# Kernel optimization log

Hardware: AMD Instinct MI355X
Metric: run time of the kernel (lower is better)

Reference implementation:

```python
import jax, jax.numpy as jnp
import numpy as np

N_NODES = 50000
N_EDGES = 800000
IN_CH = 16
OUT_CH = 16


def setup_inputs() -> dict:
    key = jax.random.key(0)
    ks = jax.random.split(key, 12)
    s = lambda d: 1.0 / np.sqrt(d)
    return {
        "x": jax.random.normal(ks[0], (N_NODES, IN_CH), jnp.float32),
        "edge_index": jax.random.randint(ks[1], (2, N_EDGES), 0, N_NODES, jnp.int64),
        "edge_attr": jax.random.uniform(ks[2], (N_EDGES, 8), jnp.float32),
        "W1": jax.random.normal(ks[3], (8, 100), jnp.float32) * s(8),
        "b1": jnp.zeros((100,), jnp.float32),
        "W2": jax.random.normal(ks[4], (100, 100), jnp.float32) * s(100),
        "b2": jnp.zeros((100,), jnp.float32),
        "W3": jax.random.normal(ks[5], (100, 100), jnp.float32) * s(100),
        "b3": jnp.zeros((100,), jnp.float32),
        "W4": jax.random.normal(ks[6], (100, IN_CH * OUT_CH), jnp.float32) * s(100),
        "b4": jnp.zeros((IN_CH * OUT_CH,), jnp.float32),
        "root": jax.random.normal(ks[7], (IN_CH, OUT_CH), jnp.float32) * s(IN_CH),
        "bias": jnp.zeros((OUT_CH,), jnp.float32),
    }


def reference(x, edge_index, edge_attr, W1, b1, W2, b2, W3, b3, W4, b4, root, bias):
    src, dst = edge_index[0], edge_index[1]
    # edge MLP -> per-edge weight matrix [E, in, out]
    h = jax.nn.relu(edge_attr @ W1 + b1)
    h = jax.nn.relu(h @ W2 + b2)
    h = jax.nn.relu(h @ W3 + b3)
    w = (h @ W4 + b4).reshape(-1, IN_CH, OUT_CH)
    # gather source features, per-edge matmul
    msg = jnp.einsum('ei,eio->eo', x[src], w)  # [E, out]
    # scatter-mean into destination nodes
    agg = jax.ops.segment_sum(msg, dst, num_segments=N_NODES)
    cnt = jax.ops.segment_sum(jnp.ones((msg.shape[0],), msg.dtype), dst, num_segments=N_NODES)
    agg = agg / jnp.maximum(cnt, 1.0)[:, None]
    return x @ root + agg + bias
```

## Files before the change

kernel.cpp:

```cpp
#include <hip/hip_runtime.h>
#include <hip/hip_bf16.h>

constexpr int N_NODES = 50000;
constexpr int E_TOTAL = 800000;
constexpr int EB   = 64;
constexpr int NT   = E_TOTAL / EB;
constexpr int GRID = 256;
constexpr int TPB  = 512;

typedef __attribute__((ext_vector_type(8))) short bf16x8;
typedef __attribute__((ext_vector_type(4))) float f32x4;

constexpr size_t WS_CNT = 0;
constexpr size_t WS_W1  = 200704;
constexpr size_t WS_W2  = WS_W1 + 8192;
constexpr size_t WS_W3  = WS_W2 + 32768;
constexpr size_t WS_W4  = WS_W3 + 32768;

constexpr int L_W4  = 0;
constexpr int L_HA  = 65536;
constexpr int L_HB  = 81920;
constexpr int L_EA  = 98304;
constexpr int L_XS  = 102400;
constexpr int L_MSG = 106496;
constexpr int L_DST = 126976;
constexpr int L_TOT = 127488;

__device__ inline unsigned short bfb(float f) {
    __hip_bfloat16 h = __float2bfloat16(f);
    return __builtin_bit_cast(unsigned short, h);
}
__device__ inline unsigned pk2(float a, float b) {
    return (unsigned)bfb(a) | ((unsigned)bfb(b) << 16);
}

__device__ inline void stage(const char* g, char* l, int bytes, int t) {
    const int wave = t >> 6, lane = t & 63;
    for (int c = wave; c * 1024 < bytes; c += 8) {
        __builtin_amdgcn_global_load_lds(
            (const __attribute__((address_space(1))) void*)(g + c * 1024 + lane * 16),
            (__attribute__((address_space(3))) void*)(l + c * 1024), 16, 0, 0);
    }
}

template<int KSTEPS, bool SWZ>
__device__ inline void layerR(char* sm, int inOff, int outOff,
                              const bf16x8 (&wf)[2][KSTEPS], const float (&bb)[2],
                              int wm, int wn, int lane)
{
    const int r16 = lane & 15, g4 = lane >> 4;
    f32x4 acc[2][2] = {};
#pragma unroll
    for (int ks = 0; ks < KSTEPS; ++ks) {
        const int kb = ks * 64 + g4 * 16;
        bf16x8 a[2];
#pragma unroll
        for (int mb = 0; mb < 2; ++mb) {
            const int r = 32 * wm + 16 * mb + r16;
            a[mb] = SWZ
                ? *reinterpret_cast<const bf16x8*>(sm + inOff + r * 256 + (kb ^ ((r & 7) << 4)))
                : *reinterpret_cast<const bf16x8*>(sm + inOff + r * 64 + kb);
        }
#pragma unroll
        for (int nf = 0; nf < 2; ++nf)
#pragma unroll
            for (int mb = 0; mb < 2; ++mb)
                acc[mb][nf] = __builtin_amdgcn_mfma_f32_16x16x32_bf16(a[mb], wf[nf][ks], acc[mb][nf], 0, 0, 0);
    }
#pragma unroll
    for (int nf = 0; nf < 2; ++nf) {
        const int n = 32 * wn + 16 * nf + r16;
#pragma unroll
        for (int mb = 0; mb < 2; ++mb)
#pragma unroll
            for (int j = 0; j < 4; ++j) {
                const int r = 32 * wm + 16 * mb + g4 * 4 + j;
                const float v = fmaxf(acc[mb][nf][j] + bb[nf], 0.f);
                *reinterpret_cast<unsigned short*>(sm + outOff + r * 256 + ((2 * n) ^ ((r & 7) << 4))) = bfb(v);
            }
    }
}

__global__ __launch_bounds__(TPB, 2)
void edge_kernel(const float* __restrict__ x, const int* __restrict__ eidx,
                 const float* __restrict__ ea,
                 const float* __restrict__ b1, const float* __restrict__ b2,
                 const float* __restrict__ b3, const float* __restrict__ b4,
                 const char* __restrict__ ws,
                 float* __restrict__ out, float* __restrict__ cnt)
{
    extern __shared__ char sm[];
    const int t    = threadIdx.x;
    const int lane = t & 63;
    const int wave = t >> 6;
    const int wm   = wave >> 2, wn = wave & 3;
    const int r16  = lane & 15, g4 = lane >> 4;

    bf16x8 wf1[2][1], wf2[2][4], wf3[2][4];
    float bb1[2], bb2[2], bb3[2], bb4[4];
#pragma unroll
    for (int nf = 0; nf < 2; ++nf) {
        const int n = 32 * wn + 16 * nf + r16;
        wf1[nf][0] = *reinterpret_cast<const bf16x8*>(ws + WS_W1 + n * 64 + g4 * 16);
#pragma unroll
        for (int ks = 0; ks < 4; ++ks) {
            wf2[nf][ks] = *reinterpret_cast<const bf16x8*>(ws + WS_W2 + n * 256 + ks * 64 + g4 * 16);
            wf3[nf][ks] = *reinterpret_cast<const bf16x8*>(ws + WS_W3 + n * 256 + ks * 64 + g4 * 16);
        }
        bb1[nf] = (n < 100) ? b1[n] : 0.f;
        bb2[nf] = (n < 100) ? b2[n] : 0.f;
        bb3[nf] = (n < 100) ? b3[n] : 0.f;
    }
#pragma unroll
    for (int nf = 0; nf < 4; ++nf) bb4[nf] = b4[64 * wn + 16 * nf + r16];

    stage(ws + WS_W4, sm + L_W4, 65536, t);

    if (t < 192) {
        const int e = t & 63, s = 1 + (t >> 6);
        *reinterpret_cast<float4*>(sm + L_EA + e * 64 + s * 16) = make_float4(0.f, 0.f, 0.f, 0.f);
    }

    float4 eaR, xvR; int dstR = 0;
    {
        const int e0 = blockIdx.x * EB;
        if (t < 128) eaR = *reinterpret_cast<const float4*>(&ea[(size_t)(e0 + (t >> 1)) * 8 + (t & 1) * 4]);
        if (t < 256) {
            const int s = eidx[e0 + (t >> 2)];
            xvR = *reinterpret_cast<const float4*>(&x[(size_t)s * 16 + (t & 3) * 4]);
        }
        if (t < 64) dstR = eidx[E_TOTAL + e0 + t];
    }
    __syncthreads();

    int parity = 0;
    for (int tile = blockIdx.x; tile < NT; tile += GRID) {
        if (t < 128) {
            const int e = t >> 1, hh = t & 1;
            uint2 pk; pk.x = pk2(eaR.x, eaR.y); pk.y = pk2(eaR.z, eaR.w);
            *reinterpret_cast<uint2*>(sm + L_EA + e * 64 + hh * 8) = pk;
        }
        if (t < 256) *reinterpret_cast<float4*>(sm + L_XS + (t >> 2) * 64 + (t & 3) * 16) = xvR;
        if (t < 64)  reinterpret_cast<int*>(sm + L_DST)[parity * 64 + t] = dstR;

        const int nxt = tile + GRID;
        if (nxt < NT) {
            const int e0 = nxt * EB;
            if (t < 128) eaR = *reinterpret_cast<const float4*>(&ea[(size_t)(e0 + (t >> 1)) * 8 + (t & 1) * 4]);
            if (t < 256) {
                const int s = eidx[e0 + (t >> 2)];
                xvR = *reinterpret_cast<const float4*>(&x[(size_t)s * 16 + (t & 3) * 4]);
            }
            if (t < 64) dstR = eidx[E_TOTAL + e0 + t];
        }
        __syncthreads();

        layerR<1, false>(sm, L_EA, L_HA, wf1, bb1, wm, wn, lane);
        __syncthreads();
        layerR<4, true >(sm, L_HA, L_HB, wf2, bb2, wm, wn, lane);
        __syncthreads();
        layerR<4, true >(sm, L_HB, L_HA, wf3, bb3, wm, wn, lane);
        __syncthreads();

        float mp[2][4] = {};
        {
            f32x4 acc[2][4] = {};
#pragma unroll
            for (int ks = 0; ks < 4; ++ks) {
                const int kb = ks * 64 + g4 * 16;
                bf16x8 a[2];
#pragma unroll
                for (int mb = 0; mb < 2; ++mb) {
                    const int r = 32 * wm + 16 * mb + r16;
                    a[mb] = *reinterpret_cast<const bf16x8*>(sm + L_HA + r * 256 + (kb ^ ((r & 7) << 4)));
                }
#pragma unroll
                for (int nf = 0; nf < 4; ++nf) {
                    const int n = 64 * wn + 16 * nf + r16;
                    const bf16x8 b = *reinterpret_cast<const bf16x8*>(sm + L_W4 + n * 256 + (kb ^ ((n & 7) << 4)));
#pragma unroll
                    for (int mb = 0; mb < 2; ++mb)
                        acc[mb][nf] = __builtin_amdgcn_mfma_f32_16x16x32_bf16(a[mb], b, acc[mb][nf], 0, 0, 0);
                }
            }
            const float* xs = reinterpret_cast<const float*>(sm + L_XS);
#pragma unroll
            for (int mb = 0; mb < 2; ++mb)
#pragma unroll
                for (int j = 0; j < 4; ++j) {
                    const int e = 32 * wm + 16 * mb + g4 * 4 + j;
                    const float4 xv = *reinterpret_cast<const float4*>(&xs[e * 16 + 4 * wn]);
#pragma unroll
                    for (int nf = 0; nf < 4; ++nf)
                        mp[mb][j] = fmaf((&xv.x)[nf], acc[mb][nf][j] + bb4[nf], mp[mb][j]);
                }
        }
        {
            float* msg = reinterpret_cast<float*>(sm + L_MSG) + wn * 1280;
#pragma unroll
            for (int mb = 0; mb < 2; ++mb)
#pragma unroll
                for (int j = 0; j < 4; ++j) {
                    const int e = 32 * wm + 16 * mb + g4 * 4 + j;
                    msg[e * 20 + r16] = mp[mb][j];
                }
        }
        __syncthreads();

        if (t < 256) {
            const int e = t >> 2, o0 = (t & 3) * 4;
            const float* m = reinterpret_cast<const float*>(sm + L_MSG);
            const float4 s0 = *reinterpret_cast<const float4*>(m + 0 * 1280 + e * 20 + o0);
            const float4 s1 = *reinterpret_cast<const float4*>(m + 1 * 1280 + e * 20 + o0);
            const float4 s2 = *reinterpret_cast<const float4*>(m + 2 * 1280 + e * 20 + o0);
            const float4 s3 = *reinterpret_cast<const float4*>(m + 3 * 1280 + e * 20 + o0);
            const int d = reinterpret_cast<const int*>(sm + L_DST)[parity * 64 + e];
            unsafeAtomicAdd(&out[(size_t)d * 16 + o0 + 0], s0.x + s1.x + s2.x + s3.x);
            unsafeAtomicAdd(&out[(size_t)d * 16 + o0 + 1], s0.y + s1.y + s2.y + s3.y);
            unsafeAtomicAdd(&out[(size_t)d * 16 + o0 + 2], s0.z + s1.z + s2.z + s3.z);
            unsafeAtomicAdd(&out[(size_t)d * 16 + o0 + 3], s0.w + s1.w + s2.w + s3.w);
            if ((t & 3) == 0) unsafeAtomicAdd(&cnt[d], 1.0f);
        }
        parity ^= 1;
    }
}

__global__ __launch_bounds__(256)
void prep_kernel(const float* __restrict__ W1, const float* __restrict__ W2,
                 const float* __restrict__ W3, const float* __restrict__ W4,
                 char* __restrict__ ws)
{
    const int id = blockIdx.x * 256 + threadIdx.x;
    if (id < N_NODES) reinterpret_cast<float*>(ws + WS_CNT)[id] = 0.f;
    if (id >= 69632) return;
    float v = 0.f;
    if (id < 4096) {
        const int n = id >> 5, k = id & 31;
        if (n < 100 && k < 8) v = W1[k * 100 + n];
        reinterpret_cast<unsigned short*>(ws + WS_W1)[id] = bfb(v);
    } else if (id < 20480) {
        const int j = id - 4096, n = j >> 7, k = j & 127;
        if (n < 100 && k < 100) v = W2[k * 100 + n];
        reinterpret_cast<unsigned short*>(ws + WS_W2)[j] = bfb(v);
    } else if (id < 36864) {
        const int j = id - 20480, n = j >> 7, k = j & 127;
        if (n < 100 && k < 100) v = W3[k * 100 + n];
        reinterpret_cast<unsigned short*>(ws + WS_W3)[j] = bfb(v);
    } else {
        const int j = id - 36864, n = j >> 7, k = j & 127;
        if (k < 100) v = W4[k * 256 + n];
        *reinterpret_cast<unsigned short*>(ws + WS_W4 + n * 256 + ((2 * k) ^ ((n & 7) << 4))) = bfb(v);
    }
}

__global__ __launch_bounds__(256)
void node_kernel(const float* __restrict__ x, const float* __restrict__ root,
                 const float* __restrict__ bias, const float* __restrict__ cnt,
                 float* __restrict__ out)
{
    const int n = blockIdx.x * blockDim.x + threadIdx.x;
    if (n >= N_NODES) return;
    float xr[16];
#pragma unroll
    for (int q = 0; q < 4; ++q) {
        const float4 v = *reinterpret_cast<const float4*>(&x[(size_t)n * 16 + 4 * q]);
        xr[4 * q] = v.x; xr[4 * q + 1] = v.y; xr[4 * q + 2] = v.z; xr[4 * q + 3] = v.w;
    }
    const float inv = 1.f / fmaxf(cnt[n], 1.f);
#pragma unroll
    for (int q = 0; q < 4; ++q) {
        float4 o4 = *reinterpret_cast<float4*>(&out[(size_t)n * 16 + 4 * q]);
        float res[4];
#pragma unroll
        for (int j = 0; j < 4; ++j) {
            const int o = 4 * q + j;
            float dot = 0.f;
#pragma unroll
            for (int i = 0; i < 16; ++i)
                dot = fmaf(xr[i], root[i * 16 + o], dot);
            res[j] = dot + (&o4.x)[j] * inv + bias[o];
        }
        *reinterpret_cast<float4*>(&out[(size_t)n * 16 + 4 * q]) = make_float4(res[0], res[1], res[2], res[3]);
    }
}

extern "C" void kernel_launch(void* const* d_in, const int* in_sizes, int n_in,
                              void* d_out, int out_size, void* d_ws, size_t ws_size,
                              hipStream_t stream)
{
    const float* x    = (const float*)d_in[0];
    const int*   eidx = (const int*)  d_in[1];
    const float* ea   = (const float*)d_in[2];
    const float* W1   = (const float*)d_in[3];
    const float* b1   = (const float*)d_in[4];
    const float* W2   = (const float*)d_in[5];
    const float* b2   = (const float*)d_in[6];
    const float* W3   = (const float*)d_in[7];
    const float* b3   = (const float*)d_in[8];
    const float* W4   = (const float*)d_in[9];
    const float* b4   = (const float*)d_in[10];
    const float* root = (const float*)d_in[11];
    const float* bias = (const float*)d_in[12];
    float* out = (float*)d_out;
    char*  ws  = (char*)d_ws;
    float* cnt = (float*)d_ws;

    (void)in_sizes; (void)n_in; (void)ws_size;

    hipFuncSetAttribute((const void*)edge_kernel,
                        hipFuncAttributeMaxDynamicSharedMemorySize, L_TOT);

    hipMemsetAsync(d_out, 0, (size_t)out_size * sizeof(float), stream);

    hipLaunchKernelGGL(prep_kernel, dim3(272), dim3(256), 0, stream, W1, W2, W3, W4, ws);
    hipLaunchKernelGGL(edge_kernel, dim3(GRID), dim3(TPB), L_TOT, stream,
                       x, eidx, ea, b1, b2, b3, b4, ws, out, cnt);
    hipLaunchKernelGGL(node_kernel, dim3((N_NODES + 255) / 256), dim3(256), 0, stream,
                       x, root, bias, cnt, out);
}
```

Baseline: 339.2 us.

## Double edge tile, fold biases into weights, transpose MFMAs, defer scatter atomics

```diff
diff --git a/kernel.cpp b/kernel.cpp
--- a/kernel.cpp
+++ b/kernel.cpp
@@ -3,7 +3,7 @@
 
 constexpr int N_NODES = 50000;
 constexpr int E_TOTAL = 800000;
-constexpr int EB   = 64;
+constexpr int EB   = 128;
 constexpr int NT   = E_TOTAL / EB;
 constexpr int GRID = 256;
 constexpr int TPB  = 512;
@@ -18,13 +18,12 @@
 constexpr size_t WS_W4  = WS_W3 + 32768;
 
 constexpr int L_W4  = 0;
-constexpr int L_HA  = 65536;
-constexpr int L_HB  = 81920;
-constexpr int L_EA  = 98304;
-constexpr int L_XS  = 102400;
-constexpr int L_MSG = 106496;
-constexpr int L_DST = 126976;
-constexpr int L_TOT = 127488;
+constexpr int L_HA  = 69632;
+constexpr int L_HB  = 104448;
+constexpr int L_EA  = 139264;
+constexpr int L_XS  = 149504;
+constexpr int L_DST = 159744;
+constexpr int L_TOT = 160768;
 
 __device__ inline unsigned short bfb(float f) {
     __hip_bfloat16 h = __float2bfloat16(f);
@@ -43,213 +42,233 @@
     }
 }
 
-template<int KSTEPS, bool SWZ>
-__device__ inline void layerR(char* sm, int inOff, int outOff,
-                              const bf16x8 (&wf)[2][KSTEPS], const float (&bb)[2],
-                              int wm, int wn, int lane)
+template<int IN_OFF, int OUT_OFF>
+__device__ inline void layerB(char* sm, const bf16x8 (&wf)[2][4],
+                              int we, int wn, int lane)
 {
     const int r16 = lane & 15, g4 = lane >> 4;
-    f32x4 acc[2][2] = {};
-#pragma unroll
-    for (int ks = 0; ks < KSTEPS; ++ks) {
-        const int kb = ks * 64 + g4 * 16;
-        bf16x8 a[2];
-#pragma unroll
-        for (int mb = 0; mb < 2; ++mb) {
-            const int r = 32 * wm + 16 * mb + r16;
-            a[mb] = SWZ
-                ? *reinterpret_cast<const bf16x8*>(sm + inOff + r * 256 + (kb ^ ((r & 7) << 4)))
-                : *reinterpret_cast<const bf16x8*>(sm + inOff + r * 64 + kb);
-        }
-#pragma unroll
-        for (int nf = 0; nf < 2; ++nf)
-#pragma unroll
-            for (int mb = 0; mb < 2; ++mb)
-                acc[mb][nf] = __builtin_amdgcn_mfma_f32_16x16x32_bf16(a[mb], wf[nf][ks], acc[mb][nf], 0, 0, 0);
-    }
-#pragma unroll
-    for (int nf = 0; nf < 2; ++nf) {
-        const int n = 32 * wn + 16 * nf + r16;
-#pragma unroll
-        for (int mb = 0; mb < 2; ++mb)
-#pragma unroll
-            for (int j = 0; j < 4; ++j) {
-                const int r = 32 * wm + 16 * mb + g4 * 4 + j;
-                const float v = fmaxf(acc[mb][nf][j] + bb[nf], 0.f);
-                *reinterpret_cast<unsigned short*>(sm + outOff + r * 256 + ((2 * n) ^ ((r & 7) << 4))) = bfb(v);
-            }
-    }
+    f32x4 acc[2][4] = {};
+#pragma unroll
+    for (int ks = 0; ks < 4; ++ks) {
+        bf16x8 b[4];
+#pragma unroll
+        for (int ef = 0; ef < 4; ++ef) {
+            const int e = 64 * we + 16 * ef + r16;
+            b[ef] = *reinterpret_cast<const bf16x8*>(sm + IN_OFF + e * 272 + ks * 64 + g4 * 16);
+        }
+#pragma unroll
+        for (int mf = 0; mf < 2; ++mf)
+#pragma unroll
+            for (int ef = 0; ef < 4; ++ef)
+                acc[mf][ef] = __builtin_amdgcn_mfma_f32_16x16x32_bf16(wf[mf][ks], b[ef], acc[mf][ef], 0, 0, 0);
+    }
+#pragma unroll
+    for (int mf = 0; mf < 2; ++mf)
+#pragma unroll
+        for (int ef = 0; ef < 4; ++ef) {
+            const int e = 64 * we + 16 * ef + r16;
+            uint2 pk;
+            pk.x = pk2(fmaxf(acc[mf][ef][0], 0.f), fmaxf(acc[mf][ef][1], 0.f));
+            pk.y = pk2(fmaxf(acc[mf][ef][2], 0.f), fmaxf(acc[mf][ef][3], 0.f));
+            *reinterpret_cast<uint2*>(sm + OUT_OFF + e * 272 + 64 * wn + 32 * mf + 8 * g4) = pk;
+        }
 }
 
 __global__ __launch_bounds__(TPB, 2)
 void edge_kernel(const float* __restrict__ x, const int* __restrict__ eidx,
-                 const float* __restrict__ ea,
-                 const float* __restrict__ b1, const float* __restrict__ b2,
-                 const float* __restrict__ b3, const float* __restrict__ b4,
-                 const char* __restrict__ ws,
+                 const float* __restrict__ ea, const char* __restrict__ ws,
                  float* __restrict__ out, float* __restrict__ cnt)
 {
     extern __shared__ char sm[];
     const int t    = threadIdx.x;
     const int lane = t & 63;
     const int wave = t >> 6;
-    const int wm   = wave >> 2, wn = wave & 3;
+    const int we   = wave >> 2, wn = wave & 3;
+    const int we4  = wave >> 1, wn4 = wave & 1;
     const int r16  = lane & 15, g4 = lane >> 4;
-
-    bf16x8 wf1[2][1], wf2[2][4], wf3[2][4];
-    float bb1[2], bb2[2], bb3[2], bb4[4];
-#pragma unroll
-    for (int nf = 0; nf < 2; ++nf) {
-        const int n = 32 * wn + 16 * nf + r16;
-        wf1[nf][0] = *reinterpret_cast<const bf16x8*>(ws + WS_W1 + n * 64 + g4 * 16);
+    int* dsti = reinterpret_cast<int*>(sm + L_DST);
+
+    bf16x8 wf1[2], wf2[2][4], wf3[2][4];
+#pragma unroll
+    for (int mf = 0; mf < 2; ++mf) {
+        const int n = 32 * wn + 16 * mf + r16;
+        wf1[mf] = *reinterpret_cast<const bf16x8*>(ws + WS_W1 + n * 64 + g4 * 16);
 #pragma unroll
         for (int ks = 0; ks < 4; ++ks) {
-            wf2[nf][ks] = *reinterpret_cast<const bf16x8*>(ws + WS_W2 + n * 256 + ks * 64 + g4 * 16);
-            wf3[nf][ks] = *reinterpret_cast<const bf16x8*>(ws + WS_W3 + n * 256 + ks * 64 + g4 * 16);
-        }
-        bb1[nf] = (n < 100) ? b1[n] : 0.f;
-        bb2[nf] = (n < 100) ? b2[n] : 0.f;
-        bb3[nf] = (n < 100) ? b3[n] : 0.f;
-    }
-#pragma unroll
-    for (int nf = 0; nf < 4; ++nf) bb4[nf] = b4[64 * wn + 16 * nf + r16];
-
-    stage(ws + WS_W4, sm + L_W4, 65536, t);
-
-    if (t < 192) {
-        const int e = t & 63, s = 1 + (t >> 6);
-        *reinterpret_cast<float4*>(sm + L_EA + e * 64 + s * 16) = make_float4(0.f, 0.f, 0.f, 0.f);
+            wf2[mf][ks] = *reinterpret_cast<const bf16x8*>(ws + WS_W2 + n * 256 + ks * 64 + g4 * 16);
+            wf3[mf][ks] = *reinterpret_cast<const bf16x8*>(ws + WS_W3 + n * 256 + ks * 64 + g4 * 16);
+        }
+    }
+
+    stage(ws + WS_W4, sm + L_W4, 69632, t);
+
+    {
+        const int e = t >> 2, q = t & 3;
+        if (q > 0) {
+            uint4 z = make_uint4(0u, 0u, 0u, 0u);
+            if (q == 1) z.x = 0x3F80u;
+            *reinterpret_cast<uint4*>(sm + L_EA + e * 80 + 16 * q) = z;
+        }
     }
 
     float4 eaR, xvR; int dstR = 0;
     {
         const int e0 = blockIdx.x * EB;
-        if (t < 128) eaR = *reinterpret_cast<const float4*>(&ea[(size_t)(e0 + (t >> 1)) * 8 + (t & 1) * 4]);
+        if (t < 256) eaR = *reinterpret_cast<const float4*>(&ea[(size_t)(e0 + (t >> 1)) * 8 + (t & 1) * 4]);
+        const int s = eidx[e0 + (t >> 2)];
+        xvR = *reinterpret_cast<const float4*>(&x[(size_t)s * 16 + (t & 3) * 4]);
+        if (t < 128) dstR = eidx[E_TOTAL + e0 + t];
+    }
+
+    int p = 0;
+    bool has_prev = false;
+    for (int tile = blockIdx.x; tile < NT; tile += GRID) {
+        if (has_prev) {
+            const int e = t >> 2, o0 = (t & 3) * 4;
+            const float4 s0 = *reinterpret_cast<const float4*>(sm + L_HB + e * 80 + o0 * 4);
+            const float4 s1 = *reinterpret_cast<const float4*>(sm + L_HB + 10240 + e * 80 + o0 * 4);
+            const int d = dsti[(p ^ 1) * 128 + e];
+            unsafeAtomicAdd(&out[(size_t)d * 16 + o0 + 0], s0.x + s1.x);
+            unsafeAtomicAdd(&out[(size_t)d * 16 + o0 + 1], s0.y + s1.y);
+            unsafeAtomicAdd(&out[(size_t)d * 16 + o0 + 2], s0.z + s1.z);
+            unsafeAtomicAdd(&out[(size_t)d * 16 + o0 + 3], s0.w + s1.w);
+            if ((t & 3) == 0) unsafeAtomicAdd(&cnt[d], 1.0f);
+        }
         if (t < 256) {
-            const int s = eidx[e0 + (t >> 2)];
-            xvR = *reinterpret_cast<const float4*>(&x[(size_t)s * 16 + (t & 3) * 4]);
-        }
-        if (t < 64) dstR = eidx[E_TOTAL + e0 + t];
-    }
-    __syncthreads();
-
-    int parity = 0;
-    for (int tile = blockIdx.x; tile < NT; tile += GRID) {
-        if (t < 128) {
-            const int e = t >> 1, hh = t & 1;
             uint2 pk; pk.x = pk2(eaR.x, eaR.y); pk.y = pk2(eaR.z, eaR.w);
-            *reinterpret_cast<uint2*>(sm + L_EA + e * 64 + hh * 8) = pk;
-        }
-        if (t < 256) *reinterpret_cast<float4*>(sm + L_XS + (t >> 2) * 64 + (t & 3) * 16) = xvR;
-        if (t < 64)  reinterpret_cast<int*>(sm + L_DST)[parity * 64 + t] = dstR;
+            *reinterpret_cast<uint2*>(sm + L_EA + (t >> 1) * 80 + 8 * (t & 1)) = pk;
+        }
+        *reinterpret_cast<float4*>(sm + L_XS + (t >> 2) * 80 + (t & 3) * 16) = xvR;
+        if (t < 128) dsti[p * 128 + t] = dstR;
 
         const int nxt = tile + GRID;
         if (nxt < NT) {
             const int e0 = nxt * EB;
-            if (t < 128) eaR = *reinterpret_cast<const float4*>(&ea[(size_t)(e0 + (t >> 1)) * 8 + (t & 1) * 4]);
-            if (t < 256) {
-                const int s = eidx[e0 + (t >> 2)];
-                xvR = *reinterpret_cast<const float4*>(&x[(size_t)s * 16 + (t & 3) * 4]);
-            }
-            if (t < 64) dstR = eidx[E_TOTAL + e0 + t];
-        }
-        __syncthreads();
-
-        layerR<1, false>(sm, L_EA, L_HA, wf1, bb1, wm, wn, lane);
-        __syncthreads();
-        layerR<4, true >(sm, L_HA, L_HB, wf2, bb2, wm, wn, lane);
-        __syncthreads();
-        layerR<4, true >(sm, L_HB, L_HA, wf3, bb3, wm, wn, lane);
-        __syncthreads();
-
-        float mp[2][4] = {};
+            if (t < 256) eaR = *reinterpret_cast<const float4*>(&ea[(size_t)(e0 + (t >> 1)) * 8 + (t & 1) * 4]);
+            const int s = eidx[e0 + (t >> 2)];
+            xvR = *reinterpret_cast<const float4*>(&x[(size_t)s * 16 + (t & 3) * 4]);
+            if (t < 128) dstR = eidx[E_TOTAL + e0 + t];
+        }
+        __syncthreads();
+
         {
             f32x4 acc[2][4] = {};
+            bf16x8 b[4];
+#pragma unroll
+            for (int ef = 0; ef < 4; ++ef) {
+                const int e = 64 * we + 16 * ef + r16;
+                b[ef] = *reinterpret_cast<const bf16x8*>(sm + L_EA + e * 80 + g4 * 16);
+            }
+#pragma unroll
+            for (int mf = 0; mf < 2; ++mf)
+#pragma unroll
+                for (int ef = 0; ef < 4; ++ef)
+                    acc[mf][ef] = __builtin_amdgcn_mfma_f32_16x16x32_bf16(wf1[mf], b[ef], acc[mf][ef], 0, 0, 0);
+#pragma unroll
+            for (int mf = 0; mf < 2; ++mf)
+#pragma unroll
+                for (int ef = 0; ef < 4; ++ef) {
+                    const int e = 64 * we + 16 * ef + r16;
+                    uint2 pk;
+                    pk.x = pk2(fmaxf(acc[mf][ef][0], 0.f), fmaxf(acc[mf][ef][1], 0.f));
+                    pk.y = pk2(fmaxf(acc[mf][ef][2], 0.f), fmaxf(acc[mf][ef][3], 0.f));
+                    *reinterpret_cast<uint2*>(sm + L_HA + e * 272 + 64 * wn + 32 * mf + 8 * g4) = pk;
+                }
+        }
+        __syncthreads();
+        layerB<L_HA, L_HB>(sm, wf2, we, wn, lane);
+        __syncthreads();
+        layerB<L_HB, L_HA>(sm, wf3, we, wn, lane);
+        __syncthreads();
+
+        {
+            f32x4 acc[8][2] = {};
 #pragma unroll
             for (int ks = 0; ks < 4; ++ks) {
-                const int kb = ks * 64 + g4 * 16;
-                bf16x8 a[2];
-#pragma unroll
-                for (int mb = 0; mb < 2; ++mb) {
-                    const int r = 32 * wm + 16 * mb + r16;
-                    a[mb] = *reinterpret_cast<const bf16x8*>(sm + L_HA + r * 256 + (kb ^ ((r & 7) << 4)));
+                bf16x8 b[2];
+#pragma unroll
+                for (int ef = 0; ef < 2; ++ef) {
+                    const int e = 32 * we4 + 16 * ef + r16;
+                    b[ef] = *reinterpret_cast<const bf16x8*>(sm + L_HA + e * 272 + ks * 64 + g4 * 16);
                 }
 #pragma unroll
-                for (int nf = 0; nf < 4; ++nf) {
-                    const int n = 64 * wn + 16 * nf + r16;
-                    const bf16x8 b = *reinterpret_cast<const bf16x8*>(sm + L_W4 + n * 256 + (kb ^ ((n & 7) << 4)));
-#pragma unroll
-                    for (int mb = 0; mb < 2; ++mb)
-                        acc[mb][nf] = __builtin_amdgcn_mfma_f32_16x16x32_bf16(a[mb], b, acc[mb][nf], 0, 0, 0);
+                for (int mf = 0; mf < 8; ++mf) {
+                    const int n = 128 * wn4 + 16 * mf + r16;
+                    const bf16x8 a = *reinterpret_cast<const bf16x8*>(sm + L_W4 + n * 272 + ks * 64 + g4 * 16);
+#pragma unroll
+                    for (int ef = 0; ef < 2; ++ef)
+                        acc[mf][ef] = __builtin_amdgcn_mfma_f32_16x16x32_bf16(a, b[ef], acc[mf][ef], 0, 0, 0);
                 }
             }
-            const float* xs = reinterpret_cast<const float*>(sm + L_XS);
-#pragma unroll
-            for (int mb = 0; mb < 2; ++mb)
-#pragma unroll
-                for (int j = 0; j < 4; ++j) {
-                    const int e = 32 * wm + 16 * mb + g4 * 4 + j;
-                    const float4 xv = *reinterpret_cast<const float4*>(&xs[e * 16 + 4 * wn]);
-#pragma unroll
-                    for (int nf = 0; nf < 4; ++nf)
-                        mp[mb][j] = fmaf((&xv.x)[nf], acc[mb][nf][j] + bb4[nf], mp[mb][j]);
+#pragma unroll
+            for (int ef = 0; ef < 2; ++ef) {
+                const int e = 32 * we4 + 16 * ef + r16;
+                const float4 xa = *reinterpret_cast<const float4*>(sm + L_XS + e * 80 + 32 * wn4);
+                const float4 xb = *reinterpret_cast<const float4*>(sm + L_XS + e * 80 + 32 * wn4 + 16);
+                float4 mp = make_float4(0.f, 0.f, 0.f, 0.f);
+#pragma unroll
+                for (int mf = 0; mf < 8; ++mf) {
+                    const float xi = (mf < 4) ? (&xa.x)[mf] : (&xb.x)[mf - 4];
+                    mp.x = fmaf(xi, acc[mf][ef][0], mp.x);
+                    mp.y = fmaf(xi, acc[mf][ef][1], mp.y);
+                    mp.z = fmaf(xi, acc[mf][ef][2], mp.z);
+                    mp.w = fmaf(xi, acc[mf][ef][3], mp.w);
                 }
-        }
-        {
-            float* msg = reinterpret_cast<float*>(sm + L_MSG) + wn * 1280;
-#pragma unroll
-            for (int mb = 0; mb < 2; ++mb)
-#pragma unroll
-                for (int j = 0; j < 4; ++j) {
-                    const int e = 32 * wm + 16 * mb + g4 * 4 + j;
-                    msg[e * 20 + r16] = mp[mb][j];
-                }
-        }
-        __syncthreads();
-
-        if (t < 256) {
-            const int e = t >> 2, o0 = (t & 3) * 4;
-            const float* m = reinterpret_cast<const float*>(sm + L_MSG);
-            const float4 s0 = *reinterpret_cast<const float4*>(m + 0 * 1280 + e * 20 + o0);
-            const float4 s1 = *reinterpret_cast<const float4*>(m + 1 * 1280 + e * 20 + o0);
-            const float4 s2 = *reinterpret_cast<const float4*>(m + 2 * 1280 + e * 20 + o0);
-            const float4 s3 = *reinterpret_cast<const float4*>(m + 3 * 1280 + e * 20 + o0);
-            const int d = reinterpret_cast<const int*>(sm + L_DST)[parity * 64 + e];
-            unsafeAtomicAdd(&out[(size_t)d * 16 + o0 + 0], s0.x + s1.x + s2.x + s3.x);
-            unsafeAtomicAdd(&out[(size_t)d * 16 + o0 + 1], s0.y + s1.y + s2.y + s3.y);
-            unsafeAtomicAdd(&out[(size_t)d * 16 + o0 + 2], s0.z + s1.z + s2.z + s3.z);
-            unsafeAtomicAdd(&out[(size_t)d * 16 + o0 + 3], s0.w + s1.w + s2.w + s3.w);
-            if ((t & 3) == 0) unsafeAtomicAdd(&cnt[d], 1.0f);
-        }
-        parity ^= 1;
+                *reinterpret_cast<float4*>(sm + L_HB + wn4 * 10240 + e * 80 + g4 * 16) = mp;
+            }
+        }
+        __syncthreads();
+        p ^= 1;
+        has_prev = true;
+    }
+
+    {
+        const int e = t >> 2, o0 = (t & 3) * 4;
+        const float4 s0 = *reinterpret_cast<const float4*>(sm + L_HB + e * 80 + o0 * 4);
+        const float4 s1 = *reinterpret_cast<const float4*>(sm + L_HB + 10240 + e * 80 + o0 * 4);
+        const int d = dsti[(p ^ 1) * 128 + e];
+        unsafeAtomicAdd(&out[(size_t)d * 16 + o0 + 0], s0.x + s1.x);
+        unsafeAtomicAdd(&out[(size_t)d * 16 + o0 + 1], s0.y + s1.y);
+        unsafeAtomicAdd(&out[(size_t)d * 16 + o0 + 2], s0.z + s1.z);
+        unsafeAtomicAdd(&out[(size_t)d * 16 + o0 + 3], s0.w + s1.w);
+        if ((t & 3) == 0) unsafeAtomicAdd(&cnt[d], 1.0f);
     }
 }
 
 __global__ __launch_bounds__(256)
-void prep_kernel(const float* __restrict__ W1, const float* __restrict__ W2,
-                 const float* __restrict__ W3, const float* __restrict__ W4,
+void prep_kernel(const float* __restrict__ W1, const float* __restrict__ b1,
+                 const float* __restrict__ W2, const float* __restrict__ b2,
+                 const float* __restrict__ W3, const float* __restrict__ b3,
+                 const float* __restrict__ W4, const float* __restrict__ b4,
                  char* __restrict__ ws)
 {
     const int id = blockIdx.x * 256 + threadIdx.x;
     if (id < N_NODES) reinterpret_cast<float*>(ws + WS_CNT)[id] = 0.f;
     if (id >= 69632) return;
-    float v = 0.f;
     if (id < 4096) {
         const int n = id >> 5, k = id & 31;
-        if (n < 100 && k < 8) v = W1[k * 100 + n];
+        float v = 0.f;
+        if (k < 8)        { if (n < 100) v = W1[k * 100 + n]; }
+        else if (k == 8)  { v = (n < 100) ? b1[n] : (n == 100 ? 1.f : 0.f); }
         reinterpret_cast<unsigned short*>(ws + WS_W1)[id] = bfb(v);
     } else if (id < 20480) {
         const int j = id - 4096, n = j >> 7, k = j & 127;
-        if (n < 100 && k < 100) v = W2[k * 100 + n];
+        float v = 0.f;
+        if (k < 100)       { if (n < 100) v = W2[k * 100 + n]; }
+        else if (k == 100) { v = (n < 100) ? b2[n] : (n == 100 ? 1.f : 0.f); }
         reinterpret_cast<unsigned short*>(ws + WS_W2)[j] = bfb(v);
     } else if (id < 36864) {
         const int j = id - 20480, n = j >> 7, k = j & 127;
-        if (n < 100 && k < 100) v = W3[k * 100 + n];
+        float v = 0.f;
+        if (k < 100)       { if (n < 100) v = W3[k * 100 + n]; }
+        else if (k == 100) { v = (n < 100) ? b3[n] : (n == 100 ? 1.f : 0.f); }
         reinterpret_cast<unsigned short*>(ws + WS_W3)[j] = bfb(v);
     } else {
         const int j = id - 36864, n = j >> 7, k = j & 127;
-        if (k < 100) v = W4[k * 256 + n];
-        *reinterpret_cast<unsigned short*>(ws + WS_W4 + n * 256 + ((2 * k) ^ ((n & 7) << 4))) = bfb(v);
+        float v = 0.f;
+        if (k < 100)       v = W4[k * 256 + n];
+        else if (k == 100) v = b4[n];
+        *reinterpret_cast<unsigned short*>(ws + WS_W4 + n * 272 + 2 * k) = bfb(v);
     }
 }
 
@@ -312,9 +331,10 @@
 
     hipMemsetAsync(d_out, 0, (size_t)out_size * sizeof(float), stream);
 
-    hipLaunchKernelGGL(prep_kernel, dim3(272), dim3(256), 0, stream, W1, W2, W3, W4, ws);
+    hipLaunchKernelGGL(prep_kernel, dim3(272), dim3(256), 0, stream,
+                       W1, b1, W2, b2, W3, b3, W4, b4, ws);
     hipLaunchKernelGGL(edge_kernel, dim3(GRID), dim3(TPB), L_TOT, stream,
-                       x, eidx, ea, b1, b2, b3, b4, ws, out, cnt);
+                       x, eidx, ea, ws, out, cnt);
     hipLaunchKernelGGL(node_kernel, dim3((N_NODES + 255) / 256), dim3(256), 0, stream,
                        x, root, bias, cnt, out);
 }
```

After: 344.5 us. About the same (+1.6%).
